# Kernel tuning notes

Hardware: AMD Instinct MI355X
Metric: run time of the kernel (lower is better)

Reference implementation:

```python
import jax, jax.numpy as jnp
import numpy as np

B, S, H = 2, 2048, 2048
NH = 16
HD = H // NH          # 128
ROT = HD // 4         # rotary_dim = head_dim * 0.25 = 32
VP = 320              # v_proj_dim
BASE = 10000.0


def setup_inputs() -> dict:
    key = jax.random.key(0)
    ks = jax.random.split(key, 10)
    sc = lambda fan_in: 1.0 / np.sqrt(fan_in)
    return {
        "hidden_states": jax.random.normal(ks[0], (B, S, H), jnp.float32),
        "Wqkv": jax.random.normal(ks[1], (3 * H, H), jnp.float32) * sc(H),
        "bqkv": jnp.zeros((3 * H,), jnp.float32),
        "Wc": jax.random.normal(ks[2], (VP, H), jnp.float32) * sc(H),
        "bc": jnp.zeros((VP,), jnp.float32),
        "Wr": jax.random.normal(ks[3], (H, VP), jnp.float32) * sc(VP),
        "br": jnp.zeros((H,), jnp.float32),
        "Wd": jax.random.normal(ks[4], (H, H), jnp.float32) * sc(H),
        "bd": jnp.zeros((H,), jnp.float32),
    }


def _rope_tables(seq_len, rot_dim, dtype):
    inv_freq = 1.0 / (BASE ** (jnp.arange(0, rot_dim, 2, dtype=jnp.float32) / rot_dim))
    t = jnp.arange(seq_len, dtype=jnp.float32)
    freqs = jnp.outer(t, inv_freq)                      # [S, rot/2]
    emb = jnp.concatenate([freqs, freqs], axis=-1)      # [S, rot]
    return jnp.cos(emb).astype(dtype), jnp.sin(emb).astype(dtype)


def _rotate_half(x):
    x1, x2 = jnp.split(x, 2, axis=-1)
    return jnp.concatenate([-x2, x1], axis=-1)


def reference(hidden_states, Wqkv, bqkv, Wc, bc, Wr, br, Wd, bd):
    b, s, h = hidden_states.shape
    qkv = hidden_states @ Wqkv.T + bqkv                 # [B,S,3H]
    qkv = qkv.reshape(b, s, 3, NH, HD)
    qkv = jnp.transpose(qkv, (2, 0, 3, 1, 4))           # [3,B,NH,S,HD]
    q, k, v = qkv[0], qkv[1], qkv[2]

    cos, sin = _rope_tables(s, ROT, hidden_states.dtype)  # [S,ROT]
    cos = cos[None, None, :, :]
    sin = sin[None, None, :, :]
    q_rot, q_pass = q[..., :ROT], q[..., ROT:]
    k_rot, k_pass = k[..., :ROT], k[..., ROT:]
    q_rot = q_rot * cos + _rotate_half(q_rot) * sin
    k_rot = k_rot * cos + _rotate_half(k_rot) * sin
    q = jnp.concatenate([q_rot, q_pass], axis=-1)
    k = jnp.concatenate([k_rot, k_pass], axis=-1)

    # V low-rank compress / restore
    v_hidden = jnp.transpose(v, (0, 2, 1, 3)).reshape(b, s, h)  # [B,S,H]
    v_restored = (v_hidden @ Wc.T + bc) @ Wr.T + br             # [B,S,H]
    v_heads = jnp.transpose(v_restored.reshape(b, s, NH, HD), (0, 2, 1, 3))  # [B,NH,S,HD]

    scale = HD ** -0.5
    scores = jnp.einsum('bhqd,bhkd->bhqk', q, k) * scale
    causal = jnp.triu(jnp.full((s, s), -jnp.inf, scores.dtype), k=1)
    scores = scores + causal
    attn = jax.nn.softmax(scores, axis=-1)
    out = jnp.einsum('bhqk,bhkd->bhqd', attn, v_heads)
    out = jnp.transpose(out, (0, 2, 1, 3)).reshape(b, s, h)
    return out @ Wd.T + bd
```

## Files before the change

kernel.cpp:

```cpp
#include <hip/hip_runtime.h>

typedef unsigned short u16;
typedef unsigned int u32;
typedef __bf16 bf16x8 __attribute__((ext_vector_type(8)));
typedef float f32x4 __attribute__((ext_vector_type(4)));

#define BB 2
#define SS 2048
#define HH 2048
#define NHH 16
#define HDD 128

__device__ __forceinline__ float b2f(u16 u) {
  union { u32 i; float f; } v; v.i = ((u32)u) << 16; return v.f;
}
__device__ __forceinline__ u16 f2b(float f) {
  union { float f; u32 i; } v; v.f = f;
  u32 x = v.i;
  u32 r = (x + 0x7fffu + ((x >> 16) & 1u)) >> 16;
  return (u16)r;
}

__device__ __forceinline__ void gload_lds16(const u16* g, u16* l) {
  __builtin_amdgcn_global_load_lds(
      (const __attribute__((address_space(1))) u32*)g,
      (__attribute__((address_space(3))) u32*)l, 16, 0, 0);
}

__global__ __launch_bounds__(256) void cvt_kernel(
    const float* __restrict__ s0, u16* __restrict__ d0, int n0,
    const float* __restrict__ s1, u16* __restrict__ d1, int n1,
    const float* __restrict__ s2, u16* __restrict__ d2, int n2,
    const float* __restrict__ s3, u16* __restrict__ d3, int n3,
    const float* __restrict__ s4, u16* __restrict__ d4, int n4)
{
  const float* s; u16* d; int n;
  switch (blockIdx.y) {
    case 0: s = s0; d = d0; n = n0; break;
    case 1: s = s1; d = d1; n = n1; break;
    case 2: s = s2; d = d2; n = n2; break;
    case 3: s = s3; d = d3; n = n3; break;
    default: s = s4; d = d4; n = n4; break;
  }
  int nq = n >> 2;
  for (int q = blockIdx.x * 256 + threadIdx.x; q < nq; q += gridDim.x * 256) {
    float4 v = *(const float4*)(s + (size_t)q * 4);
    ushort4 o;
    o.x = f2b(v.x); o.y = f2b(v.y); o.z = f2b(v.z); o.w = f2b(v.w);
    *(ushort4*)(d + (size_t)q * 4) = o;
  }
}


template<int ISA>
__device__ __forceinline__ void stage_half(
    const u16* __restrict__ src, u16* ldsmat, int h,
    int tb, int kb, int ld, int wid, int lane)
{
#pragma unroll
  for (int l = 0; l < 2; ++l) {
    const int i = wid * 2 + l;
    const int rp = i * 8 + (lane >> 3);
    int r;
    if (ISA) r = (rp & 63) + ((rp >> 6) << 7) + h * 64;
    else     r = ((rp >> 5) << 6) + h * 32 + (rp & 31);
    const int c = (lane & 7) ^ (lane >> 3);
    gload_lds16(src + (size_t)(tb + r) * ld + kb + c * 8,
                ldsmat + (size_t)(h * 128 + i * 8) * 64);
  }
}

#define BAR()   __builtin_amdgcn_s_barrier()
#define PRIO1() __builtin_amdgcn_s_setprio(1)
#define PRIO0() __builtin_amdgcn_s_setprio(0)

#define LDA_READ(BP, MH) do {                                                  \
  const u16* _p = (BP);                                                        \
  _Pragma("unroll") for (int mi = 0; mi < 4; ++mi) {                           \
    const int _rho = (MH) * 128 + wr * 64 + mi * 16 + lm;                      \
    _Pragma("unroll") for (int ks = 0; ks < 2; ++ks)                           \
      af[mi][ks] = *(const bf16x8*)&_p[(size_t)_rho * 64 +                     \
                                       ((((ks << 2) + quad) ^ (lm & 7)) << 3)];\
  }                                                                            \
} while (0)

#define LDB_READ(BP, NH) do {                                                  \
  const u16* _p = (BP);                                                        \
  _Pragma("unroll") for (int ni = 0; ni < 2; ++ni) {                           \
    const int _rho = (NH) * 128 + wc * 32 + ni * 16 + lm;                      \
    _Pragma("unroll") for (int ks = 0; ks < 2; ++ks)                           \
      bfr[NH][ni][ks] = *(const bf16x8*)&_p[(size_t)_rho * 64 +                \
                                       ((((ks << 2) + quad) ^ (lm & 7)) << 3)];\
  }                                                                            \
} while (0)

#define MFMA_Q(MH, NH) do {                                                    \
  _Pragma("unroll") for (int mi = 0; mi < 4; ++mi)                             \
    _Pragma("unroll") for (int ni = 0; ni < 2; ++ni)                           \
      _Pragma("unroll") for (int ks = 0; ks < 2; ++ks)                         \
        acc[(MH) * 4 + mi][(NH) * 2 + ni] =                                    \
            __builtin_amdgcn_mfma_f32_16x16x32_bf16(                           \
                af[mi][ks], bfr[NH][ni][ks],                                   \
                acc[(MH) * 4 + mi][(NH) * 2 + ni], 0, 0, 0);                   \
} while (0)

__global__ __launch_bounds__(512, 2) void gemm256_rope_kernel(
    const u16* __restrict__ A, const u16* __restrict__ Bw,
    const float* __restrict__ bias, u16* __restrict__ C,
    int M, int N, int K, int lda, int ldb, int ldc)
{
  __shared__ u16 lds[2][2][256 * 64];
  const int t = threadIdx.x;
  const int lane = t & 63, wid = t >> 6;
  const int wr = wid >> 2, wc = wid & 3;
  const int quad = lane >> 4, lm = lane & 15;

  const int nwg = gridDim.x * gridDim.y;
  const int lid = blockIdx.y * gridDim.x + blockIdx.x;
  const int sb = (lid & 7) * (nwg >> 3) + (lid >> 3);
  const int m0 = (sb % gridDim.y) * 256, n0 = (sb / gridDim.y) * 256;

  u16* As0 = &lds[0][0][0]; u16* Bs0 = &lds[0][1][0];
  u16* As1 = &lds[1][0][0]; u16* Bs1 = &lds[1][1][0];

  f32x4 acc[8][4] = {};
  bf16x8 af[4][2];
  bf16x8 bfr[2][2][2];

  const int NT = K >> 6;

  stage_half<1>(A,  As0, 0, m0, 0, lda, wid, lane);
  stage_half<0>(Bw, Bs0, 0, n0, 0, ldb, wid, lane);
  stage_half<0>(Bw, Bs0, 1, n0, 0, ldb, wid, lane);
  stage_half<1>(A,  As0, 1, m0, 0, lda, wid, lane);
  asm volatile("s_waitcnt vmcnt(4)" ::: "memory");
  stage_half<1>(A,  As1, 0, m0, 64, lda, wid, lane);
  stage_half<0>(Bw, Bs1, 0, n0, 64, ldb, wid, lane);
  stage_half<0>(Bw, Bs1, 1, n0, 64, ldb, wid, lane);
  asm volatile("s_waitcnt vmcnt(6)" ::: "memory");
  BAR();

  for (int it2 = 0; it2 < (NT >> 1); ++it2) {
    int kb1 = (it2 * 2 + 1) << 6;
    int kb2 = (it2 * 2 + 2) << 6; if (kb2 >= K) kb2 -= K;
    int kb3 = (it2 * 2 + 3) << 6; if (kb3 >= K) kb3 -= K;

    LDA_READ(As0, 0); LDB_READ(Bs0, 0);
    stage_half<1>(A, As1, 1, m0, kb1, lda, wid, lane);
    BAR(); PRIO1(); MFMA_Q(0, 0); PRIO0(); BAR();
    LDB_READ(Bs0, 1);
    stage_half<1>(A, As0, 0, m0, kb2, lda, wid, lane);
    BAR(); PRIO1(); MFMA_Q(0, 1); PRIO0(); BAR();
    LDA_READ(As0, 1);
    stage_half<0>(Bw, Bs0, 0, n0, kb2, ldb, wid, lane);
    BAR(); PRIO1(); MFMA_Q(1, 1); PRIO0(); BAR();
    stage_half<0>(Bw, Bs0, 1, n0, kb2, ldb, wid, lane);
    asm volatile("s_waitcnt vmcnt(6)" ::: "memory");
    BAR(); PRIO1(); MFMA_Q(1, 0); PRIO0(); BAR();
    LDA_READ(As1, 0); LDB_READ(Bs1, 0);
    stage_half<1>(A, As0, 1, m0, kb2, lda, wid, lane);
    BAR(); PRIO1(); MFMA_Q(0, 0); PRIO0(); BAR();
    LDB_READ(Bs1, 1);
    stage_half<1>(A, As1, 0, m0, kb3, lda, wid, lane);
    BAR(); PRIO1(); MFMA_Q(0, 1); PRIO0(); BAR();
    LDA_READ(As1, 1);
    stage_half<0>(Bw, Bs1, 0, n0, kb3, ldb, wid, lane);
    BAR(); PRIO1(); MFMA_Q(1, 1); PRIO0(); BAR();
    stage_half<0>(Bw, Bs1, 1, n0, kb3, ldb, wid, lane);
    asm volatile("s_waitcnt vmcnt(6)" ::: "memory");
    BAR(); PRIO1(); MFMA_Q(1, 0); PRIO0(); BAR();
  }
  asm volatile("s_waitcnt vmcnt(0)" ::: "memory");

  const int cbase = n0 + wc * 64;
  const float ropefreq = exp2f(-(float)lm * 0.8304820237218406f);
  const bool do_rope = ((wc & 1) == 0) && (cbase < 4096);
  float b0 = 0.f, b1 = 0.f;
  if (do_rope) { b0 = bias[cbase + lm]; b1 = bias[cbase + lm + 16]; }

#pragma unroll
  for (int mi8 = 0; mi8 < 8; ++mi8) {
    const int gm = m0 + wr * 128 + mi8 * 16 + quad * 4;
    int jstart = 0;
    if (do_rope) {
      jstart = 2;
      const int gn0 = cbase + lm, gn1 = gn0 + 16;
#pragma unroll
      for (int rg = 0; rg < 4; ++rg) {
        int rs = gm + rg;
        float sn, cs;
        __sincosf((float)(rs & (SS - 1)) * ropefreq, &sn, &cs);
        float x0 = acc[mi8][0][rg] + b0, x1 = acc[mi8][1][rg] + b1;
        C[(size_t)rs * ldc + gn0] = f2b(x0 * cs - x1 * sn);
        C[(size_t)rs * ldc + gn1] = f2b(x1 * cs + x0 * sn);
      }
    }
#pragma unroll
    for (int nj = 0; nj < 4; ++nj) {
      if (nj < jstart) continue;
      const int gn = cbase + nj * 16 + lm;
      if (gn < N) {
        f32x4 a = acc[mi8][nj];
        float bs = bias[gn];
#pragma unroll
        for (int rg = 0; rg < 4; ++rg)
          C[(size_t)(gm + rg) * ldc + gn] = f2b(a[rg] + bs);
      }
    }
  }
}

template<int OUT_F32, int ROPE, int BIAS_ROW>
__global__ __launch_bounds__(256) void gemm_bias_kernel(
    const u16* __restrict__ A, const u16* __restrict__ Bw,
    const float* __restrict__ bias, void* __restrict__ Cv,
    int M, int N, int K, int lda, int ldb, int ldc,
    size_t strideB, size_t strideC)
{
  __shared__ u16 Asf[128 * 4 * 8];
  __shared__ u16 Bsf[128 * 4 * 8];
  const int t = threadIdx.x;
  const int gx = gridDim.x, gy = gridDim.y;
  const int nwg = gx * gy;
  const int lid = blockIdx.y * gx + blockIdx.x;
  int sb = (nwg & 7) ? lid : (lid & 7) * (nwg >> 3) + (lid >> 3);
  const int m0 = (sb % gy) * 128;
  const int n0 = (sb / gy) * 128;
  const int lane = t & 63, wid = t >> 6;
  const int wm = (wid >> 1) * 64, wn = (wid & 1) * 64;
  const int quad = lane >> 4, lm = lane & 15;

  const u16* Bz = Bw + (size_t)blockIdx.z * strideB;

  const int r16 = lane >> 2;
  const int swz = ((lane >> 2) & 3) ^ ((lane >> 4) & 3);
  const int kc = ((lane & 3) ^ swz) * 8;
  const int fswz = (lm & 3) ^ ((lm >> 2) & 3);

  f32x4 acc[4][4] = {};

  for (int k0 = 0; k0 < K; k0 += 32) {
    __syncthreads();
#pragma unroll
    for (int it = 0; it < 2; ++it) {
      int g = wid * 2 + it;
      int r = g * 16 + r16;
      gload_lds16(A + (size_t)(m0 + r) * lda + k0 + kc, &Asf[(size_t)g * 512]);
      gload_lds16(Bz + (size_t)(n0 + r) * ldb + k0 + kc, &Bsf[(size_t)g * 512]);
    }
    __syncthreads();
    bf16x8 af[4], bf[4];
#pragma unroll
    for (int i = 0; i < 4; ++i) {
      int row = wm + i * 16 + lm;
      af[i] = *(const bf16x8*)&Asf[(size_t)(row * 4 + (quad ^ fswz)) * 8];
    }
#pragma unroll
    for (int j = 0; j < 4; ++j) {
      int row = wn + j * 16 + lm;
      bf[j] = *(const bf16x8*)&Bsf[(size_t)(row * 4 + (quad ^ fswz)) * 8];
    }
#pragma unroll
    for (int i = 0; i < 4; ++i)
#pragma unroll
      for (int j = 0; j < 4; ++j)
        acc[i][j] = __builtin_amdgcn_mfma_f32_16x16x32_bf16(af[i], bf[j], acc[i][j], 0, 0, 0);
  }

  float* Cf = (float*)Cv + (OUT_F32 ? (size_t)blockIdx.z * strideC : 0);
  u16* Cu = (u16*)Cv + (OUT_F32 ? 0 : (size_t)blockIdx.z * strideC);
  const float ropefreq = ROPE ? exp2f(-(float)lm * 0.8304820237218406f) : 0.f;
  const bool do_rope = ROPE && (wn == 0) && (n0 < 4096);

#pragma unroll
  for (int i = 0; i < 4; ++i) {
    int gm = m0 + wm + i * 16 + quad * 4;
    int jstart = 0;
    if (do_rope) {
      jstart = 2;
      int gn0 = n0 + lm, gn1 = gn0 + 16;
      float b0 = bias[gn0], b1 = bias[gn1];
#pragma unroll
      for (int rg = 0; rg < 4; ++rg) {
        int rs = gm + rg;
        float sn, cs;
        __sincosf((float)(rs & (SS - 1)) * ropefreq, &sn, &cs);
        float x0 = acc[i][0][rg] + b0, x1 = acc[i][1][rg] + b1;
        Cu[(size_t)rs * ldc + gn0] = f2b(x0 * cs - x1 * sn);
        Cu[(size_t)rs * ldc + gn1] = f2b(x1 * cs + x0 * sn);
      }
    }
#pragma unroll
    for (int j = 0; j < 4; ++j) {
      if (j < jstart) continue;
      int gn = n0 + wn + j * 16 + lm;
      if (gn < N) {
        f32x4 a = acc[i][j];
#pragma unroll
        for (int rg = 0; rg < 4; ++rg) {
          float bsv = BIAS_ROW ? bias[gm + rg] : bias[gn];
          if (OUT_F32) Cf[(size_t)(gm + rg) * ldc + gn] = a[rg] + bsv;
          else         Cu[(size_t)(gm + rg) * ldc + gn] = f2b(a[rg] + bsv);
        }
      }
    }
  }
}

__global__ __launch_bounds__(256) void attn_mfma_kernel(
    const u16* __restrict__ qkv, const u16* __restrict__ vrt, u16* __restrict__ out)
{
  __shared__ u16 Kt[64 * 16 * 8];
  __shared__ u16 Vt[8][128][8];
  __shared__ u16 Pa[4][16 * 64];

  const int t = threadIdx.x;
  const int lane = t & 63, w = t >> 6;
  const int quad = lane >> 4, lm = lane & 15;
  const int lid = blockIdx.x;
  const int sbx = (lid & 7) * 128 + (lid >> 3);
  const int bh = sbx >> 5;
  const int qt = 31 - (sbx & 31);
  const int b = bh >> 4, h = bh & 15;
  const int q0 = qt * 64;
  const int qw = q0 + w * 16;

  bf16x8 qf[4];
  {
    const u16* qsrc = qkv + (size_t)(b * SS + qw + lm) * 6144 + h * 128 + quad * 8;
#pragma unroll
    for (int dc = 0; dc < 4; ++dc) qf[dc] = *(const bf16x8*)(qsrc + dc * 32);
  }

  f32x4 Oa[8] = {};
  float m_i = -1e30f, l_i = 0.f;

  const float scale = 0.08838834764831845f;
  const int nkt = qt + 1;
  const u16* kbase = qkv + (size_t)b * SS * 6144 + 2048 + h * 128;
  const u16* vbase = vrt + (size_t)bh * 128 * 2048;
  u16* pw = &Pa[w][0];

  for (int kt = 0; kt < nkt; ++kt) {
    const int kb = kt * 64;
    __syncthreads();
#pragma unroll
    for (int it = 0; it < 4; ++it) {
      int c = t + it * 256;
      int kp = c >> 4, dq = c & 15;
      *(uint4*)&Kt[(size_t)(kp * 16 + (dq ^ (kp & 15))) * 8] =
          *(const uint4*)(kbase + (size_t)(kb + kp) * 6144 + dq * 8);
      int d = c >> 3, kq = c & 7;
      *(uint4*)&Vt[kq][d][0] =
          *(const uint4*)(vbase + (size_t)d * 2048 + kb + kq * 8);
    }
    __syncthreads();

    f32x4 sa[4] = {};
#pragma unroll
    for (int ct = 0; ct < 4; ++ct) {
#pragma unroll
      for (int dc = 0; dc < 4; ++dc) {
        bf16x8 kf = *(const bf16x8*)&Kt[(size_t)((ct * 16 + lm) * 16 +
                                                 ((dc * 4 + quad) ^ lm)) * 8];
        sa[ct] = __builtin_amdgcn_mfma_f32_16x16x32_bf16(kf, qf[dc], sa[ct], 0, 0, 0);
      }
    }
#pragma unroll
    for (int ct = 0; ct < 4; ++ct)
#pragma unroll
      for (int r = 0; r < 4; ++r) sa[ct][r] *= scale;

    if (kt == nkt - 1) {
      int qpos = qw + lm;
#pragma unroll
      for (int ct = 0; ct < 4; ++ct) {
#pragma unroll
        for (int r = 0; r < 4; ++r)
          if (kb + ct * 16 + quad * 4 + r > qpos) sa[ct][r] = -1e30f;
      }
    }

    float mx = sa[0][0];
#pragma unroll
    for (int ct = 0; ct < 4; ++ct)
#pragma unroll
      for (int r = 0; r < 4; ++r) mx = fmaxf(mx, sa[ct][r]);
    mx = fmaxf(mx, __shfl_xor(mx, 16, 64));
    mx = fmaxf(mx, __shfl_xor(mx, 32, 64));
    float mnew = fmaxf(m_i, mx);
    float alpha = __expf(m_i - mnew);
    float ssum = 0.f;
#pragma unroll
    for (int ct = 0; ct < 4; ++ct)
#pragma unroll
      for (int r = 0; r < 4; ++r) {
        float p = __expf(sa[ct][r] - mnew);
        sa[ct][r] = p;
        ssum += p;
      }
    ssum += __shfl_xor(ssum, 16, 64);
    ssum += __shfl_xor(ssum, 32, 64);
    l_i = l_i * alpha + ssum;
    m_i = mnew;

    float ar[4];
#pragma unroll
    for (int r = 0; r < 4; ++r) ar[r] = __shfl(alpha, quad * 4 + r, 64);
#pragma unroll
    for (int dt = 0; dt < 8; ++dt)
#pragma unroll
      for (int r = 0; r < 4; ++r) Oa[dt][r] *= ar[r];

#pragma unroll
    for (int ct = 0; ct < 4; ++ct) {
      uint2 pk;
      pk.x = (u32)f2b(sa[ct][0]) | ((u32)f2b(sa[ct][1]) << 16);
      pk.y = (u32)f2b(sa[ct][2]) | ((u32)f2b(sa[ct][3]) << 16);
      int u = ct * 2 + (quad >> 1);
      *(uint2*)(pw + lm * 64 + ((u ^ (lm & 7)) * 8) + (quad & 1) * 4) = pk;
    }
    bf16x8 pf0 = *(const bf16x8*)(pw + lm * 64 + ((quad ^ (lm & 7)) * 8));
    bf16x8 pf1 = *(const bf16x8*)(pw + lm * 64 + (((4 + quad) ^ (lm & 7)) * 8));

#pragma unroll
    for (int dt = 0; dt < 8; ++dt) {
      bf16x8 vf0 = *(const bf16x8*)&Vt[quad][dt * 16 + lm][0];
      bf16x8 vf1 = *(const bf16x8*)&Vt[4 + quad][dt * 16 + lm][0];
      Oa[dt] = __builtin_amdgcn_mfma_f32_16x16x32_bf16(pf0, vf0, Oa[dt], 0, 0, 0);
      Oa[dt] = __builtin_amdgcn_mfma_f32_16x16x32_bf16(pf1, vf1, Oa[dt], 0, 0, 0);
    }
  }

  float inv = 1.0f / l_i;
  float ir[4];
#pragma unroll
  for (int r = 0; r < 4; ++r) ir[r] = __shfl(inv, quad * 4 + r, 64);
  u16* dst = out + (size_t)(b * SS + qw + quad * 4) * 2048 + h * 128 + lm;
#pragma unroll
  for (int r = 0; r < 4; ++r)
#pragma unroll
    for (int dt = 0; dt < 8; ++dt)
      dst[(size_t)r * 2048 + dt * 16] = f2b(Oa[dt][r] * ir[r]);
}

extern "C" void kernel_launch(void* const* d_in, const int* in_sizes, int n_in,
                              void* d_out, int out_size, void* d_ws, size_t ws_size,
                              hipStream_t stream)
{
  (void)in_sizes; (void)n_in; (void)out_size; (void)ws_size;
  const float* X    = (const float*)d_in[0];
  const float* Wqkv = (const float*)d_in[1];
  const float* bqkv = (const float*)d_in[2];
  const float* Wc   = (const float*)d_in[3];
  const float* bc   = (const float*)d_in[4];
  const float* Wr   = (const float*)d_in[5];
  const float* br   = (const float*)d_in[6];
  const float* Wd   = (const float*)d_in[7];
  const float* bd   = (const float*)d_in[8];
  float* out = (float*)d_out;

  char* ws = (char*)d_ws;
  u16* QKV   = (u16*)(ws);
  u16* Xb    = (u16*)(ws + 50331648);
  u16* AO    = (u16*)(ws + 50331648);
  u16* Wqkvb = (u16*)(ws + 67108864);
  u16* VrT   = (u16*)(ws + 67108864);
  u16* Wcb   = (u16*)(ws + 92274688);
  u16* Wrb   = (u16*)(ws + 93585408);
  u16* Cb    = (u16*)(ws + 94896128);
  u16* Wdb   = (u16*)(ws + 97517568);

  dim3 blk(256);

  cvt_kernel<<<dim3(512, 5), blk, 0, stream>>>(
      X, Xb, 4096 * 2048,
      Wqkv, Wqkvb, 6144 * 2048,
      Wc, Wcb, 320 * 2048,
      Wr, Wrb, 2048 * 320,
      Wd, Wdb, 2048 * 2048);

  gemm256_rope_kernel<<<dim3(24, 16), dim3(512), 0, stream>>>(
      Xb, Wqkvb, bqkv, QKV, 4096, 6144, 2048, 2048, 2048, 6144);
  gemm_bias_kernel<0, 0, 0><<<dim3(3, 32), blk, 0, stream>>>(
      QKV + 4096, Wcb, bc, Cb, 4096, 320, 2048, 6144, 2048, 320, 0, 0);
  gemm_bias_kernel<0, 0, 1><<<dim3(16, 16, 2), blk, 0, stream>>>(
      Wrb, Cb, br, VrT, 2048, 2048, 320, 320, 320, 2048,
      (size_t)2048 * 320, (size_t)4194304);
  attn_mfma_kernel<<<dim3(1024), blk, 0, stream>>>(QKV, VrT, AO);
  gemm_bias_kernel<1, 0, 0><<<dim3(16, 32), blk, 0, stream>>>(
      AO, Wdb, bd, out, 4096, 2048, 2048, 2048, 2048, 2048, 0, 0);
}
```

Before: 512.8 us.

## Pair causal query tiles per block and register-prefetch next K/V tile

The attention kernel now processes two query tiles per block (tile 31-p and tile p), so every block does the same amount of causal work, and the grid shrinks from 1024 to 512 blocks. K and V tiles are loaded one step ahead into registers and written to LDS at the start of the next iteration, so global loads overlap with the MFMA and softmax work. Separately, the generic GEMM drops its XCD-aware block swizzle in favour of direct blockIdx mapping. The costs are higher register pressure from the prefetch buffers, less parallelism at launch, and possibly worse L2 locality in the GEMMs.

Result: slower. 565.0 us (+10.2%).

```diff
diff --git a/kernel.cpp b/kernel.cpp
--- a/kernel.cpp
+++ b/kernel.cpp
@@ -220,12 +220,8 @@
   __shared__ u16 Asf[128 * 4 * 8];
   __shared__ u16 Bsf[128 * 4 * 8];
   const int t = threadIdx.x;
-  const int gx = gridDim.x, gy = gridDim.y;
-  const int nwg = gx * gy;
-  const int lid = blockIdx.y * gx + blockIdx.x;
-  int sb = (nwg & 7) ? lid : (lid & 7) * (nwg >> 3) + (lid >> 3);
-  const int m0 = (sb % gy) * 128;
-  const int n0 = (sb / gy) * 128;
+  const int m0 = blockIdx.y * 128;
+  const int n0 = blockIdx.x * 128;
   const int lane = t & 63, wid = t >> 6;
   const int wm = (wid >> 1) * 64, wn = (wid & 1) * 64;
   const int quad = lane >> 4, lm = lane & 15;
@@ -318,130 +314,153 @@
   const int lane = t & 63, w = t >> 6;
   const int quad = lane >> 4, lm = lane & 15;
   const int lid = blockIdx.x;
-  const int sbx = (lid & 7) * 128 + (lid >> 3);
-  const int bh = sbx >> 5;
-  const int qt = 31 - (sbx & 31);
+  const int sbx = (lid & 7) * 64 + (lid >> 3);
+  const int bh = sbx >> 4;
+  const int pr = sbx & 15;
   const int b = bh >> 4, h = bh & 15;
-  const int q0 = qt * 64;
-  const int qw = q0 + w * 16;
-
-  bf16x8 qf[4];
-  {
-    const u16* qsrc = qkv + (size_t)(b * SS + qw + lm) * 6144 + h * 128 + quad * 8;
-#pragma unroll
-    for (int dc = 0; dc < 4; ++dc) qf[dc] = *(const bf16x8*)(qsrc + dc * 32);
-  }
-
-  f32x4 Oa[8] = {};
-  float m_i = -1e30f, l_i = 0.f;
 
   const float scale = 0.08838834764831845f;
-  const int nkt = qt + 1;
   const u16* kbase = qkv + (size_t)b * SS * 6144 + 2048 + h * 128;
   const u16* vbase = vrt + (size_t)bh * 128 * 2048;
   u16* pw = &Pa[w][0];
 
-  for (int kt = 0; kt < nkt; ++kt) {
-    const int kb = kt * 64;
-    __syncthreads();
-#pragma unroll
-    for (int it = 0; it < 4; ++it) {
-      int c = t + it * 256;
-      int kp = c >> 4, dq = c & 15;
-      *(uint4*)&Kt[(size_t)(kp * 16 + (dq ^ (kp & 15))) * 8] =
-          *(const uint4*)(kbase + (size_t)(kb + kp) * 6144 + dq * 8);
-      int d = c >> 3, kq = c & 7;
-      *(uint4*)&Vt[kq][d][0] =
-          *(const uint4*)(vbase + (size_t)d * 2048 + kb + kq * 8);
-    }
-    __syncthreads();
-
-    f32x4 sa[4] = {};
-#pragma unroll
-    for (int ct = 0; ct < 4; ++ct) {
-#pragma unroll
-      for (int dc = 0; dc < 4; ++dc) {
-        bf16x8 kf = *(const bf16x8*)&Kt[(size_t)((ct * 16 + lm) * 16 +
-                                                 ((dc * 4 + quad) ^ lm)) * 8];
-        sa[ct] = __builtin_amdgcn_mfma_f32_16x16x32_bf16(kf, qf[dc], sa[ct], 0, 0, 0);
-      }
-    }
-#pragma unroll
-    for (int ct = 0; ct < 4; ++ct)
-#pragma unroll
-      for (int r = 0; r < 4; ++r) sa[ct][r] *= scale;
-
-    if (kt == nkt - 1) {
-      int qpos = qw + lm;
+  uint4 kreg[4], vreg[4];
+
+#define ATTN_ISSUE(KB) do {                                                    \
+  _Pragma("unroll") for (int it = 0; it < 4; ++it) {                           \
+    int c = t + it * 256;                                                      \
+    int kp = c >> 4, dq = c & 15;                                              \
+    kreg[it] = *(const uint4*)(kbase + (size_t)((KB) + kp) * 6144 + dq * 8);   \
+    int d = c >> 3, kq = c & 7;                                                \
+    vreg[it] = *(const uint4*)(vbase + (size_t)d * 2048 + (KB) + kq * 8);      \
+  }                                                                            \
+} while (0)
+
+#define ATTN_WRITE() do {                                                      \
+  _Pragma("unroll") for (int it = 0; it < 4; ++it) {                           \
+    int c = t + it * 256;                                                      \
+    int kp = c >> 4, dq = c & 15;                                              \
+    *(uint4*)&Kt[(size_t)(kp * 16 + (dq ^ (kp & 15))) * 8] = kreg[it];         \
+    int d = c >> 3, kq = c & 7;                                                \
+    *(uint4*)&Vt[kq][d][0] = vreg[it];                                         \
+  }                                                                            \
+} while (0)
+
+#pragma unroll 1
+  for (int ps = 0; ps < 2; ++ps) {
+    const int qt = ps ? pr : (31 - pr);
+    const int qw = qt * 64 + w * 16;
+    const int nkt = qt + 1;
+
+    bf16x8 qf[4];
+    {
+      const u16* qsrc = qkv + (size_t)(b * SS + qw + lm) * 6144 + h * 128 + quad * 8;
+#pragma unroll
+      for (int dc = 0; dc < 4; ++dc) qf[dc] = *(const bf16x8*)(qsrc + dc * 32);
+    }
+
+    f32x4 Oa[8] = {};
+    float m_i = -1e30f, l_i = 0.f;
+
+    ATTN_ISSUE(0);
+
+#pragma unroll 1
+    for (int kt = 0; kt < nkt; ++kt) {
+      const int kb = kt * 64;
+      __syncthreads();
+      ATTN_WRITE();
+      __syncthreads();
+      if (kt + 1 < nkt) ATTN_ISSUE(kb + 64);
+
+      f32x4 sa[4] = {};
 #pragma unroll
       for (int ct = 0; ct < 4; ++ct) {
 #pragma unroll
-        for (int r = 0; r < 4; ++r)
-          if (kb + ct * 16 + quad * 4 + r > qpos) sa[ct][r] = -1e30f;
-      }
-    }
-
-    float mx = sa[0][0];
-#pragma unroll
-    for (int ct = 0; ct < 4; ++ct)
-#pragma unroll
-      for (int r = 0; r < 4; ++r) mx = fmaxf(mx, sa[ct][r]);
-    mx = fmaxf(mx, __shfl_xor(mx, 16, 64));
-    mx = fmaxf(mx, __shfl_xor(mx, 32, 64));
-    float mnew = fmaxf(m_i, mx);
-    float alpha = __expf(m_i - mnew);
-    float ssum = 0.f;
-#pragma unroll
-    for (int ct = 0; ct < 4; ++ct)
-#pragma unroll
-      for (int r = 0; r < 4; ++r) {
-        float p = __expf(sa[ct][r] - mnew);
-        sa[ct][r] = p;
-        ssum += p;
-      }
-    ssum += __shfl_xor(ssum, 16, 64);
-    ssum += __shfl_xor(ssum, 32, 64);
-    l_i = l_i * alpha + ssum;
-    m_i = mnew;
-
-    float ar[4];
-#pragma unroll
-    for (int r = 0; r < 4; ++r) ar[r] = __shfl(alpha, quad * 4 + r, 64);
-#pragma unroll
-    for (int dt = 0; dt < 8; ++dt)
-#pragma unroll
-      for (int r = 0; r < 4; ++r) Oa[dt][r] *= ar[r];
-
-#pragma unroll
-    for (int ct = 0; ct < 4; ++ct) {
-      uint2 pk;
-      pk.x = (u32)f2b(sa[ct][0]) | ((u32)f2b(sa[ct][1]) << 16);
-      pk.y = (u32)f2b(sa[ct][2]) | ((u32)f2b(sa[ct][3]) << 16);
-      int u = ct * 2 + (quad >> 1);
-      *(uint2*)(pw + lm * 64 + ((u ^ (lm & 7)) * 8) + (quad & 1) * 4) = pk;
-    }
-    bf16x8 pf0 = *(const bf16x8*)(pw + lm * 64 + ((quad ^ (lm & 7)) * 8));
-    bf16x8 pf1 = *(const bf16x8*)(pw + lm * 64 + (((4 + quad) ^ (lm & 7)) * 8));
-
-#pragma unroll
-    for (int dt = 0; dt < 8; ++dt) {
-      bf16x8 vf0 = *(const bf16x8*)&Vt[quad][dt * 16 + lm][0];
-      bf16x8 vf1 = *(const bf16x8*)&Vt[4 + quad][dt * 16 + lm][0];
-      Oa[dt] = __builtin_amdgcn_mfma_f32_16x16x32_bf16(pf0, vf0, Oa[dt], 0, 0, 0);
-      Oa[dt] = __builtin_amdgcn_mfma_f32_16x16x32_bf16(pf1, vf1, Oa[dt], 0, 0, 0);
-    }
-  }
-
-  float inv = 1.0f / l_i;
-  float ir[4];
-#pragma unroll
-  for (int r = 0; r < 4; ++r) ir[r] = __shfl(inv, quad * 4 + r, 64);
-  u16* dst = out + (size_t)(b * SS + qw + quad * 4) * 2048 + h * 128 + lm;
-#pragma unroll
-  for (int r = 0; r < 4; ++r)
-#pragma unroll
-    for (int dt = 0; dt < 8; ++dt)
-      dst[(size_t)r * 2048 + dt * 16] = f2b(Oa[dt][r] * ir[r]);
+        for (int dc = 0; dc < 4; ++dc) {
+          bf16x8 kf = *(const bf16x8*)&Kt[(size_t)((ct * 16 + lm) * 16 +
+                                                   ((dc * 4 + quad) ^ lm)) * 8];
+          sa[ct] = __builtin_amdgcn_mfma_f32_16x16x32_bf16(kf, qf[dc], sa[ct], 0, 0, 0);
+        }
+      }
+#pragma unroll
+      for (int ct = 0; ct < 4; ++ct)
+#pragma unroll
+        for (int r = 0; r < 4; ++r) sa[ct][r] *= scale;
+
+      if (kt == nkt - 1) {
+        int qpos = qw + lm;
+#pragma unroll
+        for (int ct = 0; ct < 4; ++ct) {
+#pragma unroll
+          for (int r = 0; r < 4; ++r)
+            if (kb + ct * 16 + quad * 4 + r > qpos) sa[ct][r] = -1e30f;
+        }
+      }
+
+      float mx = sa[0][0];
+#pragma unroll
+      for (int ct = 0; ct < 4; ++ct)
+#pragma unroll
+        for (int r = 0; r < 4; ++r) mx = fmaxf(mx, sa[ct][r]);
+      mx = fmaxf(mx, __shfl_xor(mx, 16, 64));
+      mx = fmaxf(mx, __shfl_xor(mx, 32, 64));
+      float mnew = fmaxf(m_i, mx);
+      float alpha = __expf(m_i - mnew);
+      float ssum = 0.f;
+#pragma unroll
+      for (int ct = 0; ct < 4; ++ct)
+#pragma unroll
+        for (int r = 0; r < 4; ++r) {
+          float p = __expf(sa[ct][r] - mnew);
+          sa[ct][r] = p;
+          ssum += p;
+        }
+      ssum += __shfl_xor(ssum, 16, 64);
+      ssum += __shfl_xor(ssum, 32, 64);
+      l_i = l_i * alpha + ssum;
+      m_i = mnew;
+
+      float ar[4];
+#pragma unroll
+      for (int r = 0; r < 4; ++r) ar[r] = __shfl(alpha, quad * 4 + r, 64);
+#pragma unroll
+      for (int dt = 0; dt < 8; ++dt)
+#pragma unroll
+        for (int r = 0; r < 4; ++r) Oa[dt][r] *= ar[r];
+
+#pragma unroll
+      for (int ct = 0; ct < 4; ++ct) {
+        uint2 pk;
+        pk.x = (u32)f2b(sa[ct][0]) | ((u32)f2b(sa[ct][1]) << 16);
+        pk.y = (u32)f2b(sa[ct][2]) | ((u32)f2b(sa[ct][3]) << 16);
+        int u = ct * 2 + (quad >> 1);
+        *(uint2*)(pw + lm * 64 + ((u ^ (lm & 7)) * 8) + (quad & 1) * 4) = pk;
+      }
+      bf16x8 pf0 = *(const bf16x8*)(pw + lm * 64 + ((quad ^ (lm & 7)) * 8));
+      bf16x8 pf1 = *(const bf16x8*)(pw + lm * 64 + (((4 + quad) ^ (lm & 7)) * 8));
+
+#pragma unroll
+      for (int dt = 0; dt < 8; ++dt) {
+        bf16x8 vf0 = *(const bf16x8*)&Vt[quad][dt * 16 + lm][0];
+        bf16x8 vf1 = *(const bf16x8*)&Vt[4 + quad][dt * 16 + lm][0];
+        Oa[dt] = __builtin_amdgcn_mfma_f32_16x16x32_bf16(pf0, vf0, Oa[dt], 0, 0, 0);
+        Oa[dt] = __builtin_amdgcn_mfma_f32_16x16x32_bf16(pf1, vf1, Oa[dt], 0, 0, 0);
+      }
+    }
+
+    float inv = 1.0f / l_i;
+    float ir[4];
+#pragma unroll
+    for (int r = 0; r < 4; ++r) ir[r] = __shfl(inv, quad * 4 + r, 64);
+    u16* dst = out + (size_t)(b * SS + qw + quad * 4) * 2048 + h * 128 + lm;
+#pragma unroll
+    for (int r = 0; r < 4; ++r)
+#pragma unroll
+      for (int dt = 0; dt < 8; ++dt)
+        dst[(size_t)r * 2048 + dt * 16] = f2b(Oa[dt][r] * ir[r]);
+  }
+#undef ATTN_ISSUE
+#undef ATTN_WRITE
 }
 
 extern "C" void kernel_launch(void* const* d_in, const int* in_sizes, int n_in,
@@ -487,7 +506,7 @@
   gemm_bias_kernel<0, 0, 1><<<dim3(16, 16, 2), blk, 0, stream>>>(
       Wrb, Cb, br, VrT, 2048, 2048, 320, 320, 320, 2048,
       (size_t)2048 * 320, (size_t)4194304);
-  attn_mfma_kernel<<<dim3(1024), blk, 0, stream>>>(QKV, VrT, AO);
+  attn_mfma_kernel<<<dim3(512), blk, 0, stream>>>(QKV, VrT, AO);
   gemm_bias_kernel<1, 0, 0><<<dim3(16, 32), blk, 0, stream>>>(
       AO, Wdb, bd, out, 4096, 2048, 2048, 2048, 2048, 2048, 0, 0);
 }
```
